# Kernel tuning notes

Measured on AMD Instinct MI355X. Metric: run time of the kernel, lower is better.

## Reference

```python
import jax, jax.numpy as jnp
import numpy as np

EMB = 384
GROUPS = 4
B, T = 32, 1024
MAX_DUR = 8
SILENCE_VAL = -11.5129251


def setup_inputs() -> dict:
    key = jax.random.key(0)
    k1, k2, k3, k4, k5 = jax.random.split(key, 5)
    phoneme = jax.random.normal(k1, (B, T, EMB), dtype=jnp.float32)
    durations = jax.random.randint(k2, (B, T + 1), 0, MAX_DUR, dtype=jnp.int32)
    t_out = int(np.asarray(jnp.sum(durations, axis=-1)).max())
    silence_token = jnp.full((EMB,), SILENCE_VAL, dtype=jnp.float32)
    # DurationPredictor params (grouped conv -> ReLU -> 1x1 conv to scalar)
    conv1_w = jax.random.normal(k3, (EMB, EMB // GROUPS, 3), dtype=jnp.float32) * 0.05
    conv1_b = jnp.zeros((EMB,), dtype=jnp.float32)
    conv2_w = jax.random.normal(k4, (1, EMB, 1), dtype=jnp.float32) * 0.05
    conv2_b = jnp.zeros((1,), dtype=jnp.float32)
    return {
        "phoneme": phoneme,
        "silence_token": silence_token,
        "conv1_w": conv1_w,
        "conv1_b": conv1_b,
        "conv2_w": conv2_w,
        "conv2_b": conv2_b,
        "durations": durations,
        "t_out": t_out,
    }


def _duration_predictor(x, conv1_w, conv1_b, conv2_w, conv2_b):
    # x: [B, Tp, E] -> durations_pred [B, Tp]
    xc = jnp.transpose(x, (0, 2, 1))  # [B, E, Tp]
    h = jax.lax.conv_general_dilated(
        xc, conv1_w, window_strides=(1,), padding=((1, 1),),
        dimension_numbers=("NCH", "OIH", "NCH"), feature_group_count=GROUPS)
    h = jax.nn.relu(h + conv1_b[None, :, None])
    d = jax.lax.conv_general_dilated(
        h, conv2_w, window_strides=(1,), padding=((0, 0),),
        dimension_numbers=("NCH", "OIH", "NCH"))
    return d[:, 0, :] + conv2_b[0]  # [B, Tp]


def _regulate(phoneme, durations, t_out):
    # Equivalent to the one-hot mask matmul: frame t gets token j where
    # cumsum[j-1] <= t < cumsum[j]; frames past total length are zero.
    cum = jnp.cumsum(durations, axis=-1)  # [B, Tp]
    pos = jnp.arange(t_out, dtype=cum.dtype)  # [t_out]
    idx = jax.vmap(lambda c: jnp.searchsorted(c, pos, side="right"))(cum)  # [B, t_out]
    valid = pos[None, :] < cum[:, -1:]
    idx = jnp.clip(idx, 0, phoneme.shape[1] - 1)
    gathered = jnp.take_along_axis(phoneme, idx[..., None], axis=1)  # [B, t_out, E]
    return jnp.where(valid[..., None], gathered, jnp.zeros((), phoneme.dtype))


def reference(phoneme, silence_token, conv1_w, conv1_b, conv2_w, conv2_b, durations, t_out):
    Bn = phoneme.shape[0]
    silence = jnp.broadcast_to(silence_token[None, None, :], (Bn, 1, phoneme.shape[2]))
    ph = jnp.concatenate((phoneme, silence), axis=1)  # [B, T+1, E]
    durations_pred = _duration_predictor(ph, conv1_w, conv1_b, conv2_w, conv2_b)
    expanded = _regulate(ph, durations, t_out)  # [B, t_out, E]
    return expanded, durations_pred
```

## Files before the change

kernel.cpp:

```cpp
#include <hip/hip_runtime.h>

#define BATCH 32
#define T_IN 1024
#define TP 1025
#define EMB 384
#define GROUPS 4
#define GC 96

typedef __attribute__((ext_vector_type(8))) short short8;
typedef __attribute__((ext_vector_type(4))) float f32x4;

#define N_WPACK (GROUPS * 9 * 6 * 64 * 8)

__device__ __forceinline__ unsigned short f2bf(float f) {
    union { float f; unsigned u; } v; v.f = f;
    unsigned u = v.u + 0x7fffu + ((v.u >> 16) & 1u);
    return (unsigned short)(u >> 16);
}

__global__ __launch_bounds__(256) void prep_kernel(const float* __restrict__ w1,
                                                   unsigned short* __restrict__ wpack) {
    int i = blockIdx.x * 256 + threadIdx.x;
    if (i >= N_WPACK) return;
    int j = i & 7;
    int lane = (i >> 3) & 63;
    int rest = i >> 9;
    int nt = rest % 6; rest /= 6;
    int ks = rest % 9;
    int g = rest / 9;
    int oc = nt * 16 + (lane & 15);
    int kk = ks * 32 + (lane >> 4) * 8 + j;
    int k = kk / 96, ic = kk % 96;
    wpack[i] = f2bf(w1[((size_t)(g * GC + oc) * GC + ic) * 3 + k]);
}

__global__ __launch_bounds__(256) void scan_scatter_kernel(const int* __restrict__ dur,
                                                           unsigned short* __restrict__ idx,
                                                           int t_out) {
    const int b = blockIdx.x;
    const int tid = threadIdx.x;
    __shared__ int scum[TP];

    if (tid < 64) {
        const int* d = dur + b * TP;
        int offset = 0;
        for (int r = 0; r < 17; ++r) {
            int i2 = r * 64 + tid;
            int v = (i2 < TP) ? d[i2] : 0;
            int s = v;
#pragma unroll
            for (int off = 1; off < 64; off <<= 1) {
                int n = __shfl_up(s, off, 64);
                if (tid >= off) s += n;
            }
            if (i2 < TP) scum[i2] = s + offset;
            offset += __shfl(s, 63, 64);
        }
    }
    __syncthreads();

    unsigned short* ib = idx + (size_t)b * t_out;
    for (int j = tid; j < TP; j += 256) {
        int c = scum[j];
        int d = dur[b * TP + j];
        for (int f = c - d; f < c; ++f) ib[f] = (unsigned short)j;
    }
    const int total = scum[TP - 1];
    for (int t = total + tid; t < t_out; t += 256) ib[t] = 0xFFFFu;
}

__global__ __launch_bounds__(256) void conv_mfma_kernel(const float* __restrict__ phoneme,
                                                        const float* __restrict__ silence,
                                                        const float* __restrict__ b1,
                                                        const float* __restrict__ w2,
                                                        const float* __restrict__ b2,
                                                        const unsigned short* __restrict__ wpack,
                                                        float* __restrict__ pred) {
    const int tile = blockIdx.x;
    const int b = blockIdx.y;
    const int t0 = tile * 64;

    __shared__ __align__(16) unsigned short xs[66][392];
    __shared__ float red[4][64];

    const int tid = threadIdx.x;

    for (int e = tid; e < 66 * 96; e += 256) {
        int row = e / 96;
        int v = e - row * 96;
        int r = t0 - 1 + row;
        float4 val;
        if (r < 0 || r > T_IN) {
            val = make_float4(0.f, 0.f, 0.f, 0.f);
        } else if (r == T_IN) {
            val = *(const float4*)(silence + v * 4);
        } else {
            val = *(const float4*)(phoneme + ((size_t)(b * T_IN + r)) * EMB + v * 4);
        }
        ushort4 pk;
        pk.x = f2bf(val.x); pk.y = f2bf(val.y); pk.z = f2bf(val.z); pk.w = f2bf(val.w);
        *(ushort4*)&xs[row][v * 4] = pk;
    }
    __syncthreads();

    const int g = tid >> 6;
    const int lane = tid & 63;
    const int quad = lane >> 4;
    const int lr = lane & 15;

    f32x4 acc[4][6];
#pragma unroll
    for (int mt = 0; mt < 4; ++mt)
#pragma unroll
        for (int nt = 0; nt < 6; ++nt) acc[mt][nt] = (f32x4){0.f, 0.f, 0.f, 0.f};

    const unsigned short* wg = wpack + (size_t)g * 9 * 6 * 512;

#pragma unroll
    for (int ks = 0; ks < 9; ++ks) {
        const int tap = ks / 3;
        const int col = g * GC + 32 * (ks % 3) + quad * 8;
        short8 a[4];
#pragma unroll
        for (int mt = 0; mt < 4; ++mt)
            a[mt] = *(const short8*)&xs[mt * 16 + lr + tap][col];
#pragma unroll
        for (int nt = 0; nt < 6; ++nt) {
            short8 bf = *(const short8*)(wg + ((size_t)(ks * 6 + nt) * 64 + lane) * 8);
#pragma unroll
            for (int mt = 0; mt < 4; ++mt)
                acc[mt][nt] = __builtin_amdgcn_mfma_f32_16x16x32_bf16(a[mt], bf, acc[mt][nt], 0, 0, 0);
        }
    }

    float s[4][4];
#pragma unroll
    for (int mt = 0; mt < 4; ++mt)
#pragma unroll
        for (int reg = 0; reg < 4; ++reg) s[mt][reg] = 0.f;
#pragma unroll
    for (int nt = 0; nt < 6; ++nt) {
        int oc = g * GC + nt * 16 + lr;
        float bias = b1[oc];
        float wc = w2[oc];
#pragma unroll
        for (int mt = 0; mt < 4; ++mt)
#pragma unroll
            for (int reg = 0; reg < 4; ++reg) {
                float h = acc[mt][nt][reg] + bias;
                h = h > 0.f ? h : 0.f;
                s[mt][reg] += wc * h;
            }
    }
#pragma unroll
    for (int off = 1; off < 16; off <<= 1)
#pragma unroll
        for (int mt = 0; mt < 4; ++mt)
#pragma unroll
            for (int reg = 0; reg < 4; ++reg)
                s[mt][reg] += __shfl_xor(s[mt][reg], off, 64);
#pragma unroll
    for (int mt = 0; mt < 4; ++mt)
#pragma unroll
        for (int reg = 0; reg < 4; ++reg)
            if (lr == mt * 4 + reg) red[g][mt * 16 + quad * 4 + reg] = s[mt][reg];
    __syncthreads();

    if (tid < 64) {
        int t = t0 + tid;
        if (t < TP)
            pred[b * TP + t] = red[0][tid] + red[1][tid] + red[2][tid] + red[3][tid] + b2[0];
    }
}

__global__ __launch_bounds__(256) void gather_kernel(const float* __restrict__ phoneme,
                                                     const float* __restrict__ silence,
                                                     const unsigned short* __restrict__ idx,
                                                     float* __restrict__ out,
                                                     int t_out) {
    const int b = blockIdx.y;
    const int nfe = t_out * 96;
    int e = blockIdx.x * 256 + threadIdx.x;
    if (e >= nfe) return;
    int fl = e / 96;
    int v = e - fl * 96;
    unsigned short id = idx[(size_t)b * t_out + fl];
    float4 val;
    if (id == 0xFFFFu) {
        val = make_float4(0.f, 0.f, 0.f, 0.f);
    } else if (id == T_IN) {
        val = ((const float4*)silence)[v];
    } else {
        val = ((const float4*)phoneme)[((size_t)b * T_IN + id) * 96 + v];
    }
    ((float4*)out)[(size_t)b * nfe + e] = val;
}

extern "C" void kernel_launch(void* const* d_in, const int* in_sizes, int n_in,
                              void* d_out, int out_size, void* d_ws, size_t ws_size,
                              hipStream_t stream) {
    const float* phoneme = (const float*)d_in[0];
    const float* silence = (const float*)d_in[1];
    const float* conv1_w = (const float*)d_in[2];
    const float* conv1_b = (const float*)d_in[3];
    const float* conv2_w = (const float*)d_in[4];
    const float* conv2_b = (const float*)d_in[5];
    const int* durations = (const int*)d_in[6];
    const int t_out = (out_size - BATCH * TP) / (BATCH * EMB);

    float* out_expanded = (float*)d_out;
    float* out_pred = (float*)d_out + (size_t)BATCH * t_out * EMB;

    unsigned short* idx = (unsigned short*)d_ws;
    size_t idx_bytes = ((size_t)BATCH * t_out * sizeof(unsigned short) + 255) & ~(size_t)255;
    unsigned short* wpack = (unsigned short*)((char*)d_ws + idx_bytes);

    prep_kernel<<<(N_WPACK + 255) / 256, 256, 0, stream>>>(conv1_w, wpack);
    scan_scatter_kernel<<<BATCH, 256, 0, stream>>>(durations, idx, t_out);
    conv_mfma_kernel<<<dim3(17, BATCH), 256, 0, stream>>>(
        phoneme, silence, conv1_b, conv2_w, conv2_b, wpack, out_pred);
    gather_kernel<<<dim3((t_out * 96 + 255) / 256, BATCH), 256, 0, stream>>>(
        phoneme, silence, idx, out_expanded, t_out);
}
```

Before: 275.0 us.

## Merge weight-prep and scan kernels; widen gather to two vectors with nontemporal stores

Folds the weight-packing kernel and the duration-scan kernel into a single launch by splitting the grid between the two jobs. The scatter now reads the previous prefix sum from shared memory instead of reloading durations from global. The gather kernel handles two float4s per thread and writes them with nontemporal stores, aiming to cut launch overhead, halve the thread count and reduce cache pollution from the large output write. The early return in the prep blocks is safe because those blocks never reach a barrier.

```diff
diff --git a/kernel.cpp b/kernel.cpp
--- a/kernel.cpp
+++ b/kernel.cpp
@@ -11,6 +11,7 @@
 typedef __attribute__((ext_vector_type(4))) float f32x4;
 
 #define N_WPACK (GROUPS * 9 * 6 * 64 * 8)
+#define PREP_BLOCKS ((N_WPACK + 255) / 256)
 
 __device__ __forceinline__ unsigned short f2bf(float f) {
     union { float f; unsigned u; } v; v.f = f;
@@ -18,29 +19,31 @@
     return (unsigned short)(u >> 16);
 }
 
-__global__ __launch_bounds__(256) void prep_kernel(const float* __restrict__ w1,
-                                                   unsigned short* __restrict__ wpack) {
-    int i = blockIdx.x * 256 + threadIdx.x;
-    if (i >= N_WPACK) return;
-    int j = i & 7;
-    int lane = (i >> 3) & 63;
-    int rest = i >> 9;
-    int nt = rest % 6; rest /= 6;
-    int ks = rest % 9;
-    int g = rest / 9;
-    int oc = nt * 16 + (lane & 15);
-    int kk = ks * 32 + (lane >> 4) * 8 + j;
-    int k = kk / 96, ic = kk % 96;
-    wpack[i] = f2bf(w1[((size_t)(g * GC + oc) * GC + ic) * 3 + k]);
-}
-
-__global__ __launch_bounds__(256) void scan_scatter_kernel(const int* __restrict__ dur,
-                                                           unsigned short* __restrict__ idx,
-                                                           int t_out) {
-    const int b = blockIdx.x;
+__global__ __launch_bounds__(256) void prep_scan_kernel(const float* __restrict__ w1,
+                                                        const int* __restrict__ dur,
+                                                        unsigned short* __restrict__ wpack,
+                                                        unsigned short* __restrict__ idx,
+                                                        int t_out) {
+    __shared__ int scum[TP];
     const int tid = threadIdx.x;
-    __shared__ int scum[TP];
-
+
+    if (blockIdx.x < PREP_BLOCKS) {
+        int i = blockIdx.x * 256 + tid;
+        if (i >= N_WPACK) return;
+        int j = i & 7;
+        int lane = (i >> 3) & 63;
+        int rest = i >> 9;
+        int nt = rest % 6; rest /= 6;
+        int ks = rest % 9;
+        int g = rest / 9;
+        int oc = nt * 16 + (lane & 15);
+        int kk = ks * 32 + (lane >> 4) * 8 + j;
+        int k = kk / 96, ic = kk % 96;
+        wpack[i] = f2bf(w1[((size_t)(g * GC + oc) * GC + ic) * 3 + k]);
+        return;
+    }
+
+    const int b = blockIdx.x - PREP_BLOCKS;
     if (tid < 64) {
         const int* d = dur + b * TP;
         int offset = 0;
@@ -62,8 +65,8 @@
     unsigned short* ib = idx + (size_t)b * t_out;
     for (int j = tid; j < TP; j += 256) {
         int c = scum[j];
-        int d = dur[b * TP + j];
-        for (int f = c - d; f < c; ++f) ib[f] = (unsigned short)j;
+        int lo = j ? scum[j - 1] : 0;
+        for (int f = lo; f < c; ++f) ib[f] = (unsigned short)j;
     }
     const int total = scum[TP - 1];
     for (int t = total + tid; t < t_out; t += 256) ib[t] = 0xFFFFu;
@@ -180,20 +183,25 @@
                                                      int t_out) {
     const int b = blockIdx.y;
     const int nfe = t_out * 96;
-    int e = blockIdx.x * 256 + threadIdx.x;
+    int e = (blockIdx.x * 256 + threadIdx.x) * 2;
     if (e >= nfe) return;
     int fl = e / 96;
     int v = e - fl * 96;
     unsigned short id = idx[(size_t)b * t_out + fl];
-    float4 val;
+    f32x4 v0, v1;
     if (id == 0xFFFFu) {
-        val = make_float4(0.f, 0.f, 0.f, 0.f);
+        v0 = (f32x4){0.f, 0.f, 0.f, 0.f};
+        v1 = v0;
     } else if (id == T_IN) {
-        val = ((const float4*)silence)[v];
+        const f32x4* s4 = (const f32x4*)silence;
+        v0 = s4[v]; v1 = s4[v + 1];
     } else {
-        val = ((const float4*)phoneme)[((size_t)b * T_IN + id) * 96 + v];
-    }
-    ((float4*)out)[(size_t)b * nfe + e] = val;
+        const f32x4* p = (const f32x4*)phoneme + ((size_t)b * T_IN + id) * 96 + v;
+        v0 = p[0]; v1 = p[1];
+    }
+    f32x4* o = (f32x4*)out + (size_t)b * nfe + e;
+    __builtin_nontemporal_store(v0, o);
+    __builtin_nontemporal_store(v1, o + 1);
 }
 
 extern "C" void kernel_launch(void* const* d_in, const int* in_sizes, int n_in,
@@ -215,10 +223,10 @@
     size_t idx_bytes = ((size_t)BATCH * t_out * sizeof(unsigned short) + 255) & ~(size_t)255;
     unsigned short* wpack = (unsigned short*)((char*)d_ws + idx_bytes);
 
-    prep_kernel<<<(N_WPACK + 255) / 256, 256, 0, stream>>>(conv1_w, wpack);
-    scan_scatter_kernel<<<BATCH, 256, 0, stream>>>(durations, idx, t_out);
+    prep_scan_kernel<<<PREP_BLOCKS + BATCH, 256, 0, stream>>>(
+        conv1_w, durations, wpack, idx, t_out);
     conv_mfma_kernel<<<dim3(17, BATCH), 256, 0, stream>>>(
         phoneme, silence, conv1_b, conv2_w, conv2_b, wpack, out_pred);
-    gather_kernel<<<dim3((t_out * 96 + 255) / 256, BATCH), 256, 0, stream>>>(
+    gather_kernel<<<dim3((t_out * 96 / 2 + 255) / 256, BATCH), 256, 0, stream>>>(
         phoneme, silence, idx, out_expanded, t_out);
 }
```

Measured after the change: 295.6 us. 7.5% more time.
